# Kernel tuning notes

Hardware: AMD Instinct MI355X
Metric: run time of the kernel (lower is better)

Reference implementation:

```python
import jax, jax.numpy as jnp
import numpy as np

D_MODEL = 1024
NHEAD = 16
HEAD_DIM = D_MODEL // NHEAD
B, S = 8, 1024
NEG = -1e9  # finite stand-in for -inf (same softmax result, grad-safe)


def setup_inputs() -> dict:
    key = jax.random.key(0)
    ks = jax.random.split(key, 12)
    sc = 1.0 / np.sqrt(D_MODEL)
    inp = {
        "q": jax.random.normal(ks[0], (B, S, D_MODEL), jnp.float32),
        "k": jax.random.normal(ks[1], (B, S, D_MODEL), jnp.float32),
        "v": jax.random.normal(ks[2], (B, S, D_MODEL), jnp.float32),
        "padding_mask": jax.random.bernoulli(ks[3], 0.1, (B, S)),
        "causal_mask": jnp.where(jnp.tril(jnp.ones((S, S), bool)), 0.0, NEG).astype(jnp.float32),
        "wq": jax.random.normal(ks[4], (D_MODEL, D_MODEL), jnp.float32) * sc,
        "bq": jax.random.normal(ks[5], (D_MODEL,), jnp.float32) * sc,
        "wk": jax.random.normal(ks[6], (D_MODEL, D_MODEL), jnp.float32) * sc,
        "wv": jax.random.normal(ks[7], (D_MODEL, D_MODEL), jnp.float32) * sc,
        "bv": jax.random.normal(ks[8], (D_MODEL,), jnp.float32) * sc,
        "wo": jax.random.normal(ks[9], (D_MODEL, D_MODEL), jnp.float32) * sc,
        "bo": jax.random.normal(ks[10], (D_MODEL,), jnp.float32) * sc,
    }
    return inp


def reference(q, k, v, padding_mask, causal_mask, wq, bq, wk, wv, bv, wo, bo):
    b = q.shape[0]
    # projections (torch Linear: x @ W.T + b); k_linear has no bias
    qp = q @ wq.T + bq
    kp = k @ wk.T
    vp = v @ wv.T + bv
    # [B, S, H, Dh] -> [B, H, S, Dh]
    qh = qp.reshape(b, -1, NHEAD, HEAD_DIM).transpose(0, 2, 1, 3)
    kh = kp.reshape(b, -1, NHEAD, HEAD_DIM).transpose(0, 2, 1, 3)
    vh = vp.reshape(b, -1, NHEAD, HEAD_DIM).transpose(0, 2, 1, 3)
    scores = jnp.einsum("bhqd,bhkd->bhqk", qh, kh) / np.sqrt(HEAD_DIM).astype(np.float32)
    scores = jnp.where(padding_mask[:, None, None, :], NEG, scores)
    scores = scores + causal_mask[None, None, :, :]
    attn = jax.nn.softmax(scores, axis=-1)
    out = jnp.einsum("bhqk,bhkd->bhqd", attn, vh)
    out = out.transpose(0, 2, 1, 3).reshape(b, -1, D_MODEL)
    return out @ wo.T + bo
```

## Files before the change

kernel.cpp:

```cpp
#include <hip/hip_runtime.h>
#include <hip/hip_bf16.h>
#include <cstdint>
#include <math.h>


typedef __bf16 bf16_t;
typedef __bf16 bf16x8 __attribute__((ext_vector_type(8)));
typedef __bf16 bf16x4 __attribute__((ext_vector_type(4)));
typedef float  f32x4  __attribute__((ext_vector_type(4)));

#define MFMA16(a, b, c) __builtin_amdgcn_mfma_f32_16x16x32_bf16((a), (b), (c), 0, 0, 0)
#define NEGV (-1e9f)

__device__ __forceinline__ void gl_lds16(const void* gp, void* lp) {
  __builtin_amdgcn_global_load_lds(
      (__attribute__((address_space(1))) void*)(gp),
      (__attribute__((address_space(3))) void*)(lp), 16, 0, 0);
}

__device__ __forceinline__ void bar() {
  asm volatile("" ::: "memory");
  __builtin_amdgcn_s_barrier();
  asm volatile("" ::: "memory");
}

__device__ __forceinline__ unsigned int pk2(float lo, float hi) {
  unsigned short a = __builtin_bit_cast(unsigned short, (bf16_t)lo);
  unsigned short b = __builtin_bit_cast(unsigned short, (bf16_t)hi);
  return (unsigned int)a | ((unsigned int)b << 16);
}

__device__ __forceinline__ void cvt_body(const float* __restrict__ in,
                                         bf16_t* __restrict__ out, int i) {
  const float4* p = reinterpret_cast<const float4*>(in) + (size_t)i * 2;
  float4 a = p[0], b = p[1];
  bf16x8 r = {(bf16_t)a.x, (bf16_t)a.y, (bf16_t)a.z, (bf16_t)a.w,
              (bf16_t)b.x, (bf16_t)b.y, (bf16_t)b.z, (bf16_t)b.w};
  *reinterpret_cast<bf16x8*>(out + (size_t)i * 8) = r;
}

__global__ __launch_bounds__(256) void cvt_all(
    const float* __restrict__ q, const float* __restrict__ k, const float* __restrict__ v,
    const float* __restrict__ wq, const float* __restrict__ wk,
    const float* __restrict__ wv, const float* __restrict__ wo,
    bf16_t* __restrict__ oq, bf16_t* __restrict__ ok, bf16_t* __restrict__ ov,
    bf16_t* __restrict__ owq, bf16_t* __restrict__ owk,
    bf16_t* __restrict__ owv, bf16_t* __restrict__ owo) {
  const int bid = (int)blockIdx.x;
  if (bid < 12288) {
    const int s = bid >> 12;
    const int i = (bid & 4095) * 256 + (int)threadIdx.x;
    cvt_body(s == 0 ? q : (s == 1 ? k : v),
             s == 0 ? oq : (s == 1 ? ok : ov), i);
  } else {
    const int r = bid - 12288;
    const int s = r >> 9;
    const int i = (r & 511) * 256 + (int)threadIdx.x;
    cvt_body(s == 0 ? wq : (s == 1 ? wk : (s == 2 ? wv : wo)),
             s == 0 ? owq : (s == 1 ? owk : (s == 2 ? owv : owo)), i);
  }
}


#define GEMM_KLOOP(Ag, Wg, lds, acc, lr, lg, wr, wc)                          \
  auto stageA = [&](int buf, int tile) {                                      \
    char* dst = lds + buf * 32768 + t * 16;                                   \
    const size_t kt = (size_t)tile * 64;                                      \
    gl_lds16(Ag + kt,                    dst);                                \
    gl_lds16(Ag + kt + (size_t)64 * K,   dst + 8192);                         \
    gl_lds16(Ag + kt + (size_t)128 * K,  dst + 16384);                        \
    gl_lds16(Ag + kt + (size_t)192 * K,  dst + 24576);                        \
  };                                                                          \
  auto stageB = [&](int buf, int tile) {                                      \
    char* dst = lds + 98304 + buf * 16384 + t * 16;                           \
    const size_t kt = (size_t)tile * 64;                                      \
    gl_lds16(Wg + kt,                    dst);                                \
    gl_lds16(Wg + kt + (size_t)64 * K,   dst + 8192);                         \
  };                                                                          \
  stageA(0, 0); stageB(0, 0); stageA(1, 1); stageB(1, 1);                     \
  asm volatile("s_waitcnt vmcnt(6)" ::: "memory");   \
  bar();                                                      \
  const int xorv = (lr & 7) << 4;                                             \
  const int k0o = lg * 16, k1o = 64 + lg * 16;                                \
  for (int T = 0; T < 16; ++T) {                                              \
    const int cur = T % 3;                                                    \
    const char* Ab = lds + cur * 32768;                                       \
    const char* Bb = lds + 98304 + cur * 16384;                               \
    bf16x8 af[4][2], b0[2][2], b1[2][2];                                      \
                                \
    _Pragma("unroll")                                                         \
    for (int mt = 0; mt < 4; mt++) {                                          \
      const int row = wr * 64 + mt * 16 + lr;                                 \
      af[mt][0] = *(const bf16x8*)(Ab + row * 128 + (k0o ^ xorv));            \
      af[mt][1] = *(const bf16x8*)(Ab + row * 128 + (k1o ^ xorv));            \
    }                                                                         \
    _Pragma("unroll")                                                         \
    for (int nt = 0; nt < 2; nt++) {                                          \
      const int row = wc * 64 + nt * 16 + lr;                                 \
      b0[nt][0] = *(const bf16x8*)(Bb + row * 128 + (k0o ^ xorv));            \
      b0[nt][1] = *(const bf16x8*)(Bb + row * 128 + (k1o ^ xorv));            \
    }                                                                         \
    if (T + 2 < 16) stageA((T + 2) % 3, T + 2);                               \
    bar();                                                                    \
    asm volatile("s_waitcnt lgkmcnt(0)" ::: "memory");                        \
    __builtin_amdgcn_s_setprio(1);                                            \
    _Pragma("unroll")                                                         \
    for (int mt = 0; mt < 4; mt++)                                            \
      _Pragma("unroll")                                                       \
      for (int nt = 0; nt < 2; nt++) {                                        \
        acc[mt][nt] = MFMA16(af[mt][0], b0[nt][0], acc[mt][nt]);              \
        acc[mt][nt] = MFMA16(af[mt][1], b0[nt][1], acc[mt][nt]);              \
      }                                                                       \
    __builtin_amdgcn_s_setprio(0);                                            \
    bar();                                                                    \
            \
    _Pragma("unroll")                                                         \
    for (int nt = 0; nt < 2; nt++) {                                          \
      const int row = wc * 64 + (nt + 2) * 16 + lr;                           \
      b1[nt][0] = *(const bf16x8*)(Bb + row * 128 + (k0o ^ xorv));            \
      b1[nt][1] = *(const bf16x8*)(Bb + row * 128 + (k1o ^ xorv));            \
    }                                                                         \
    if (T + 2 < 16) stageB((T + 2) % 3, T + 2);                               \
    if (T < 14)       asm volatile("s_waitcnt vmcnt(6)" ::: "memory");        \
    else if (T == 14) asm volatile("s_waitcnt vmcnt(0)" ::: "memory");        \
    bar();                                     \
    asm volatile("s_waitcnt lgkmcnt(0)" ::: "memory");                        \
    __builtin_amdgcn_s_setprio(1);                                            \
    _Pragma("unroll")                                                         \
    for (int mt = 0; mt < 4; mt++)                                            \
      _Pragma("unroll")                                                       \
      for (int nt = 0; nt < 2; nt++) {                                        \
        acc[mt][nt + 2] = MFMA16(af[mt][0], b1[nt][0], acc[mt][nt + 2]);      \
        acc[mt][nt + 2] = MFMA16(af[mt][1], b1[nt][1], acc[mt][nt + 2]);      \
      }                                                                       \
    __builtin_amdgcn_s_setprio(0);                                            \
    bar();                                                                    \
  }

__global__ __launch_bounds__(512) void gemm_qkv(const bf16_t* __restrict__ qbf,
                                                const bf16_t* __restrict__ kbf,
                                                const bf16_t* __restrict__ vbf,
                                                const bf16_t* __restrict__ wqb,
                                                const bf16_t* __restrict__ wkb,
                                                const bf16_t* __restrict__ wvb,
                                                const float* __restrict__ bq,
                                                const float* __restrict__ bv,
                                                bf16_t* __restrict__ qp,
                                                bf16_t* __restrict__ kp,
                                                bf16_t* __restrict__ vtw) {
  __shared__ __align__(16) char lds[147456];
  const int bid = (int)blockIdx.x;
  const int z = bid >> 8;
  const int idx = bid & 255;
  const int p = ((idx >> 6) << 3) | (idx & 7);
  const int n = (idx >> 3) & 7;
  const bf16_t* A = z == 0 ? qbf : (z == 1 ? kbf : vbf);
  const bf16_t* W = z == 0 ? wqb : (z == 1 ? wkb : wvb);
  const int t = threadIdx.x;
  const int w = t >> 6, l = t & 63, lr = l & 15, lg = l >> 4;
  const int wr = w >> 1, wc = w & 1;
  const int m0 = p * 256, n0 = n * 128;
  const int K = 1024, N = 1024;

  const int gc = (t & 7) ^ ((t >> 3) & 7);
  const bf16_t* Ag = A + (size_t)(m0 + (t >> 3)) * K + gc * 8;
  const bf16_t* Wg = W + (size_t)(n0 + (t >> 3)) * K + gc * 8;

  f32x4 acc[4][4] = {};
  GEMM_KLOOP(Ag, Wg, lds, acc, lr, lg, wr, wc)

  if (z != 2) {
    bf16_t* outp = (z == 0) ? qp : kp;
    const float sc = (z == 0) ? 0.125f : 1.0f;
#pragma unroll
    for (int nt = 0; nt < 4; nt++) {
      const int col = n0 + wc * 64 + nt * 16 + lr;
      const float bb = (z == 0) ? bq[col] : 0.0f;
#pragma unroll
      for (int mt = 0; mt < 4; mt++)
#pragma unroll
        for (int i = 0; i < 4; i++) {
          const int row = m0 + wr * 64 + mt * 16 + lg * 4 + i;
          outp[(size_t)row * N + col] = (bf16_t)((acc[mt][nt][i] + bb) * sc);
        }
    }
  } else {
    __syncthreads();
    char* Tl = lds;
#pragma unroll
    for (int nt = 0; nt < 4; nt++) {
      const int col_l = wc * 64 + nt * 16 + lr;
      const float bb = bv[n0 + col_l];
#pragma unroll
      for (int mt = 0; mt < 4; mt++)
#pragma unroll
        for (int i = 0; i < 4; i++) {
          const int row_l = wr * 64 + mt * 16 + lg * 4 + i;
          *(bf16_t*)(Tl + col_l * 512 + ((row_l * 2) ^ ((col_l & 7) << 4))) =
              (bf16_t)(acc[mt][nt][i] + bb);
        }
    }
    __syncthreads();
    const int b = m0 >> 10, s0 = m0 & 1023;
    const int c_l = t >> 2, sub = t & 3;
    bf16_t* dst = vtw + (size_t)(b * 1024 + n0 + c_l) * 1024 + s0 + sub * 64;
    const char* Trow = Tl + c_l * 512;
    const int sw2 = (c_l & 7) << 4;
#pragma unroll
    for (int jj = 0; jj < 8; jj++) {
      const int lc = sub * 8 + jj;
      bf16x8 vv = *(const bf16x8*)(Trow + ((lc << 4) ^ sw2));
      *(bf16x8*)(dst + jj * 8) = vv;
    }
  }
}

__global__ __launch_bounds__(512) void gemm_out(const bf16_t* __restrict__ A,
                                                const bf16_t* __restrict__ W,
                                                const float* __restrict__ bias,
                                                float* __restrict__ outp) {
  __shared__ __align__(16) char lds[147456];
  const int bid = (int)blockIdx.x;
  const int p = ((bid >> 6) << 3) | (bid & 7);
  const int n = (bid >> 3) & 7;
  const int t = threadIdx.x;
  const int w = t >> 6, l = t & 63, lr = l & 15, lg = l >> 4;
  const int wr = w >> 1, wc = w & 1;
  const int m0 = p * 256, n0 = n * 128;
  const int K = 1024, N = 1024;

  const int gc = (t & 7) ^ ((t >> 3) & 7);
  const bf16_t* Ag = A + (size_t)(m0 + (t >> 3)) * K + gc * 8;
  const bf16_t* Wg = W + (size_t)(n0 + (t >> 3)) * K + gc * 8;

  f32x4 acc[4][4] = {};
  GEMM_KLOOP(Ag, Wg, lds, acc, lr, lg, wr, wc)

#pragma unroll
  for (int nt = 0; nt < 4; nt++) {
    const int col = n0 + wc * 64 + nt * 16 + lr;
    const float bb = bias[col];
#pragma unroll
    for (int mt = 0; mt < 4; mt++)
#pragma unroll
      for (int i = 0; i < 4; i++) {
        const int row = m0 + wr * 64 + mt * 16 + lg * 4 + i;
        outp[(size_t)row * N + col] = acc[mt][nt][i] + bb;
      }
  }
}

__device__ __forceinline__ void pack_bfly(const f32x4 (&s)[4], int lg,
                                          bf16x8& pbv0, bf16x8& pbv1) {
  unsigned int u[4][2], sh[4][2];
#pragma unroll
  for (int nt = 0; nt < 4; nt++) {
    u[nt][0] = pk2(s[nt][0], s[nt][1]);
    u[nt][1] = pk2(s[nt][2], s[nt][3]);
  }
#pragma unroll
  for (int nt = 0; nt < 4; nt++) {
    sh[nt][0] = (unsigned int)__shfl_xor((int)u[nt][0], 16, 64);
    sh[nt][1] = (unsigned int)__shfl_xor((int)u[nt][1], 16, 64);
  }
  const bool ev = (lg & 1) == 0;
  unsigned int Y[8];
  Y[0] = ev ? u[0][0] : sh[1][0];  Y[1] = ev ? u[0][1] : sh[1][1];
  Y[2] = ev ? u[2][0] : sh[3][0];  Y[3] = ev ? u[2][1] : sh[3][1];
  Y[4] = ev ? sh[0][0] : u[1][0];  Y[5] = ev ? sh[0][1] : u[1][1];
  Y[6] = ev ? sh[2][0] : u[3][0];  Y[7] = ev ? sh[2][1] : u[3][1];
  const bool mid = (lg == 1) || (lg == 2);
#pragma unroll
  for (int j = 0; j < 8; j++) {
    const unsigned int z = (unsigned int)__shfl_xor((int)Y[j], 48, 64);
    Y[j] = mid ? z : Y[j];
  }
  union U8 { unsigned int u[4]; bf16x8 v; };
  U8 p0, p1;
  p0.u[0] = Y[0]; p0.u[1] = Y[1]; p0.u[2] = Y[4]; p0.u[3] = Y[5];
  p1.u[0] = Y[2]; p1.u[1] = Y[3]; p1.u[2] = Y[6]; p1.u[3] = Y[7];
  pbv0 = p0.v;
  pbv1 = p1.v;
}

__global__ __launch_bounds__(512, 8) void attn_fused(const bf16_t* __restrict__ qp,
                                                     const bf16_t* __restrict__ kp,
                                                     const bf16_t* __restrict__ vt,
                                                     const int* __restrict__ pad,
                                                     bf16_t* __restrict__ outp) {
  __shared__ bf16_t Ks[2][64 * 64];
  __shared__ bf16_t Vts[2][64 * 64];
  __shared__ int padI[1024];
  __shared__ int sfl[8], sfh[8];
  const int t = threadIdx.x, w = t >> 6, l = t & 63, lr = l & 15, lg = l >> 4;
  const int L = (int)blockIdx.x;
  const int bh = (L & 7) + ((L >> 6) << 3);
  const int j = (L >> 3) & 7;
  const int b = bh >> 4, h = bh & 15;
  const int lo = j, hi = 15 - j;

  const int srow = t >> 3, sc = t & 7;
  const int gc = sc ^ (srow & 7);
  const bf16_t* kgb = kp + (size_t)(b * 1024 + srow) * 1024 + h * 64 + gc * 8;
  const bf16_t* vgb = vt + (size_t)(bh * 64 + srow) * 1024 + gc * 8;

  auto stage = [&](int bufi, int k0s) {
    gl_lds16(kgb + (size_t)k0s * 1024, (char*)(Ks[bufi]) + t * 16);
    gl_lds16(vgb + k0s,                (char*)(Vts[bufi]) + t * 16);
  };

  bool unl = false, unh = false;
  for (int jj = t; jj <= hi * 64; jj += 512) {
    const bool u = (pad[b * 1024 + jj] == 0);
    unh |= u;
    unl |= (u && (jj <= lo * 64));
  }
  const bool al = __any(unl), ah = __any(unh);
  if (l == 0) { sfl[w] = al ? 1 : 0; sfh[w] = ah ? 1 : 0; }

  stage(0, 0);
  if (t < 256) gl_lds16(pad + b * 1024 + t * 4, (char*)padI + t * 16);

  const int mytile = (w < 4) ? hi : lo;
  const int qrow_l = mytile * 64 + (w & 3) * 16 + lr;
  const int base16 = mytile * 64 + (w & 3) * 16;
  const bf16_t* qg = qp + (size_t)(b * 1024 + qrow_l) * 1024 + h * 64 + lg * 8;
  const bf16x8 qa0 = *reinterpret_cast<const bf16x8*>(qg);
  const bf16x8 qa1 = *reinterpret_cast<const bf16x8*>(qg + 32);

  __syncthreads();
  int ul = 0, uh = 0;
#pragma unroll
  for (int i = 0; i < 8; i++) { ul |= sfl[i]; uh |= sfh[i]; }
  const bool mydeg = (w < 4) ? (uh == 0) : (ul == 0);
  const int ktEnd = (ul == 0) ? 16 : (hi + 1);

  f32x4 o[4] = {};
  float m_ = -INFINITY, ld_ = 0.0f;

  for (int kt = 0; kt < ktEnd; ++kt) {
    const int cur = kt & 1;
    if (kt + 1 < ktEnd) {
      stage(cur ^ 1, (kt + 1) * 64);
      asm volatile("s_waitcnt vmcnt(2)" ::: "memory");
    } else {
      asm volatile("s_waitcnt vmcnt(0)" ::: "memory");
    }
    __builtin_amdgcn_s_barrier();

    if (kt <= mytile || mydeg) {
      const char* Kb = (const char*)(Ks[cur]);
      const char* Vb = (const char*)(Vts[cur]);
      const int k0 = kt * 64;

      f32x4 s[4] = {};
#pragma unroll
      for (int nt = 0; nt < 4; nt++) {
        const int row = nt * 16 + lr;
        const int sw = (row & 7) << 4;
        bf16x8 kb0 = *reinterpret_cast<const bf16x8*>(Kb + row * 128 + ((lg * 16) ^ sw));
        bf16x8 kb1 = *reinterpret_cast<const bf16x8*>(Kb + row * 128 + ((lg * 16 + 64) ^ sw));
        s[nt] = MFMA16(kb0, qa0, s[nt]);
        s[nt] = MFMA16(kb1, qa1, s[nt]);
      }

      const bool nc = (k0 + 63 > base16);
#pragma unroll
      for (int nt = 0; nt < 4; nt++) {
        const int kc4 = k0 + nt * 16 + lg * 4;
        const int4 pd = *reinterpret_cast<const int4*>(&padI[kc4]);
        const int pdv[4] = {pd.x, pd.y, pd.z, pd.w};
#pragma unroll
        for (int i = 0; i < 4; i++) {
          float v = s[nt][i];
          if (pdv[i]) v = NEGV;
          if (nc && (kc4 + i > qrow_l)) v += NEGV;
          s[nt][i] = v;
        }
      }

      float mx = s[0][0];
#pragma unroll
      for (int nt = 0; nt < 4; nt++)
#pragma unroll
        for (int i = 0; i < 4; i++) mx = fmaxf(mx, s[nt][i]);
      mx = fmaxf(mx, __shfl_xor(mx, 16, 64));
      mx = fmaxf(mx, __shfl_xor(mx, 32, 64));

      if (!__all(mx <= m_ - 88.0f)) {
        if (!__all(mx <= m_ + 8.0f)) {
          const float mn = fmaxf(m_, mx);
          const float scl = __expf(m_ - mn);
          m_ = mn;
          ld_ *= scl;
#pragma unroll
          for (int nt = 0; nt < 4; nt++) o[nt] *= scl;
        }
        float a = 0.0f;
#pragma unroll
        for (int nt = 0; nt < 4; nt++)
#pragma unroll
          for (int i = 0; i < 4; i++) {
            const float p = __expf(s[nt][i] - m_);
            s[nt][i] = p;
            a += p;
          }
        a += __shfl_xor(a, 16, 64);
        a += __shfl_xor(a, 32, 64);
        ld_ += a;

        bf16x8 pb0, pb1;
        pack_bfly(s, lg, pb0, pb1);

#pragma unroll
        for (int nt = 0; nt < 4; nt++) {
          const int vrow = nt * 16 + lr;
          const int vsw = (vrow & 7) << 4;
          bf16x8 vf0 = *reinterpret_cast<const bf16x8*>(Vb + vrow * 128 + ((lg * 16) ^ vsw));
          bf16x8 vf1 = *reinterpret_cast<const bf16x8*>(Vb + vrow * 128 + ((64 + lg * 16) ^ vsw));
          o[nt] = MFMA16(vf0, pb0, o[nt]);
          o[nt] = MFMA16(vf1, pb1, o[nt]);
        }
      }
    }
    __builtin_amdgcn_s_barrier();
  }

  const float rinv = 1.0f / ld_;
#pragma unroll
  for (int nt = 0; nt < 4; nt++) {
    bf16x4 rr = {(bf16_t)(o[nt][0] * rinv), (bf16_t)(o[nt][1] * rinv),
                 (bf16_t)(o[nt][2] * rinv), (bf16_t)(o[nt][3] * rinv)};
    *reinterpret_cast<bf16x4*>(outp + (size_t)(b * 1024 + qrow_l) * 1024 + h * 64 + nt * 16 + lg * 4) = rr;
  }
}

extern "C" void kernel_launch(void* const* d_in, const int* in_sizes, int n_in,
                              void* d_out, int out_size, void* d_ws, size_t ws_size,
                              hipStream_t stream) {
  const float* q   = (const float*)d_in[0];
  const float* k   = (const float*)d_in[1];
  const float* v   = (const float*)d_in[2];
  const int*   pad = (const int*)d_in[3];
  const float* wq  = (const float*)d_in[5];
  const float* bq  = (const float*)d_in[6];
  const float* wk  = (const float*)d_in[7];
  const float* wv  = (const float*)d_in[8];
  const float* bv  = (const float*)d_in[9];
  const float* wo  = (const float*)d_in[10];
  const float* bo  = (const float*)d_in[11];

  char* ws = (char*)d_ws;
  const size_t MiB = 1024 * 1024;
  bf16_t* qbf = (bf16_t*)(ws + 0 * MiB);
  bf16_t* kbf = (bf16_t*)(ws + 16 * MiB);
  bf16_t* vbf = (bf16_t*)(ws + 32 * MiB);
  bf16_t* qp  = (bf16_t*)(ws + 48 * MiB);
  bf16_t* kp  = (bf16_t*)(ws + 64 * MiB);
  bf16_t* vtw = (bf16_t*)(ws + 80 * MiB);
  bf16_t* wqb = (bf16_t*)(ws + 96 * MiB);
  bf16_t* wkb = (bf16_t*)(ws + 98 * MiB);
  bf16_t* wvb = (bf16_t*)(ws + 100 * MiB);
  bf16_t* wob = (bf16_t*)(ws + 102 * MiB);
  bf16_t* attnO = qbf;

  cvt_all<<<14336, 256, 0, stream>>>(q, k, v, wq, wk, wv, wo,
                                     qbf, kbf, vbf, wqb, wkb, wvb, wob);

  gemm_qkv<<<768, 512, 0, stream>>>(qbf, kbf, vbf, wqb, wkb, wvb, bq, bv, qp, kp, vtw);

  attn_fused<<<1024, 512, 0, stream>>>(qp, kp, vtw, pad, attnO);

  gemm_out<<<256, 512, 0, stream>>>(attnO, wob, bo, (float*)d_out);
}
```

Before: 174.1 us.

## Fuse fp32-to-bf16 activation conversion into QKV projection GEMM A-loads

Result: slower. 191.1 us (+9.7%).

```diff
diff --git a/kernel.cpp b/kernel.cpp
--- a/kernel.cpp
+++ b/kernel.cpp
@@ -39,55 +39,99 @@
   *reinterpret_cast<bf16x8*>(out + (size_t)i * 8) = r;
 }
 
-__global__ __launch_bounds__(256) void cvt_all(
-    const float* __restrict__ q, const float* __restrict__ k, const float* __restrict__ v,
+__global__ __launch_bounds__(256) void cvt_w(
     const float* __restrict__ wq, const float* __restrict__ wk,
     const float* __restrict__ wv, const float* __restrict__ wo,
-    bf16_t* __restrict__ oq, bf16_t* __restrict__ ok, bf16_t* __restrict__ ov,
     bf16_t* __restrict__ owq, bf16_t* __restrict__ owk,
     bf16_t* __restrict__ owv, bf16_t* __restrict__ owo) {
   const int bid = (int)blockIdx.x;
-  if (bid < 12288) {
-    const int s = bid >> 12;
-    const int i = (bid & 4095) * 256 + (int)threadIdx.x;
-    cvt_body(s == 0 ? q : (s == 1 ? k : v),
-             s == 0 ? oq : (s == 1 ? ok : ov), i);
-  } else {
-    const int r = bid - 12288;
-    const int s = r >> 9;
-    const int i = (r & 511) * 256 + (int)threadIdx.x;
-    cvt_body(s == 0 ? wq : (s == 1 ? wk : (s == 2 ? wv : wo)),
-             s == 0 ? owq : (s == 1 ? owk : (s == 2 ? owv : owo)), i);
-  }
-}
-
-
-#define GEMM_KLOOP(Ag, Wg, lds, acc, lr, lg, wr, wc)                          \
-  auto stageA = [&](int buf, int tile) {                                      \
-    char* dst = lds + buf * 32768 + t * 16;                                   \
-    const size_t kt = (size_t)tile * 64;                                      \
-    gl_lds16(Ag + kt,                    dst);                                \
-    gl_lds16(Ag + kt + (size_t)64 * K,   dst + 8192);                         \
-    gl_lds16(Ag + kt + (size_t)128 * K,  dst + 16384);                        \
-    gl_lds16(Ag + kt + (size_t)192 * K,  dst + 24576);                        \
-  };                                                                          \
-  auto stageB = [&](int buf, int tile) {                                      \
-    char* dst = lds + 98304 + buf * 16384 + t * 16;                           \
-    const size_t kt = (size_t)tile * 64;                                      \
-    gl_lds16(Wg + kt,                    dst);                                \
-    gl_lds16(Wg + kt + (size_t)64 * K,   dst + 8192);                         \
-  };                                                                          \
-  stageA(0, 0); stageB(0, 0); stageA(1, 1); stageB(1, 1);                     \
-  asm volatile("s_waitcnt vmcnt(6)" ::: "memory");   \
-  bar();                                                      \
-  const int xorv = (lr & 7) << 4;                                             \
-  const int k0o = lg * 16, k1o = 64 + lg * 16;                                \
-  for (int T = 0; T < 16; ++T) {                                              \
-    const int cur = T % 3;                                                    \
-    const char* Ab = lds + cur * 32768;                                       \
-    const char* Bb = lds + 98304 + cur * 16384;                               \
+  const int s = bid >> 9;
+  const int i = (bid & 511) * 256 + (int)threadIdx.x;
+  cvt_body(s == 0 ? wq : (s == 1 ? wk : (s == 2 ? wv : wo)),
+           s == 0 ? owq : (s == 1 ? owk : (s == 2 ? owv : owo)), i);
+}
+
+
+struct AReg { float4 v[8]; };
+
+__device__ __forceinline__ void loadA_f32(const float* __restrict__ Agf,
+                                          int tile, AReg& g) {
+  const size_t kt = (size_t)tile * 64;
+#pragma unroll
+  for (int rr = 0; rr < 4; rr++) {
+    const float* src = Agf + (size_t)(rr * 64) * 1024 + kt;
+    g.v[rr * 2]     = *(const float4*)(src);
+    g.v[rr * 2 + 1] = *(const float4*)(src + 4);
+  }
+}
+
+__device__ __forceinline__ void cvtWriteA(char* ldsA, int t, const AReg& g) {
+#pragma unroll
+  for (int rr = 0; rr < 4; rr++) {
+    float4 a = g.v[rr * 2], b = g.v[rr * 2 + 1];
+    bf16x8 r = {(bf16_t)a.x, (bf16_t)a.y, (bf16_t)a.z, (bf16_t)a.w,
+                (bf16_t)b.x, (bf16_t)b.y, (bf16_t)b.z, (bf16_t)b.w};
+    *(bf16x8*)(ldsA + rr * 8192 + t * 16) = r;
+  }
+}
+
+__global__ __launch_bounds__(512) void gemm_qkv(const float* __restrict__ qf,
+                                                const float* __restrict__ kf,
+                                                const float* __restrict__ vf,
+                                                const bf16_t* __restrict__ wqb,
+                                                const bf16_t* __restrict__ wkb,
+                                                const bf16_t* __restrict__ wvb,
+                                                const float* __restrict__ bq,
+                                                const float* __restrict__ bv,
+                                                bf16_t* __restrict__ qp,
+                                                bf16_t* __restrict__ kp,
+                                                bf16_t* __restrict__ vtw) {
+  __shared__ __align__(16) char lds[114688];
+  const int bid = (int)blockIdx.x;
+  const int z = bid >> 8;
+  const int idx = bid & 255;
+  const int p = ((idx >> 6) << 3) | (idx & 7);
+  const int n = (idx >> 3) & 7;
+  const float*  A = z == 0 ? qf : (z == 1 ? kf : vf);
+  const bf16_t* W = z == 0 ? wqb : (z == 1 ? wkb : wvb);
+  const int t = threadIdx.x;
+  const int w = t >> 6, l = t & 63, lr = l & 15, lg = l >> 4;
+  const int wr = w >> 1, wc = w & 1;
+  const int m0 = p * 256, n0 = n * 128;
+  const int K = 1024, N = 1024;
+
+  const int gc = (t & 7) ^ ((t >> 3) & 7);
+  const float*  Agf = A + (size_t)(m0 + (t >> 3)) * K + gc * 8;
+  const bf16_t* Wg  = W + (size_t)(n0 + (t >> 3)) * K + gc * 8;
+
+  auto stageB = [&](int buf, int tile) {
+    char* dst = lds + 65536 + buf * 16384 + t * 16;
+    const size_t kt = (size_t)tile * 64;
+    gl_lds16(Wg + kt,                  dst);
+    gl_lds16(Wg + kt + (size_t)64 * K, dst + 8192);
+  };
+
+  AReg g0, g1;
+  loadA_f32(Agf, 0, g0);
+  stageB(0, 0);
+  loadA_f32(Agf, 1, g1);
+  stageB(1, 1);
+  asm volatile("s_waitcnt vmcnt(12)" ::: "memory");
+  cvtWriteA(lds, t, g0);
+  asm volatile("s_waitcnt vmcnt(10)" ::: "memory");
+  asm volatile("s_waitcnt lgkmcnt(0)" ::: "memory");
+  bar();
+
+  f32x4 acc[4][4] = {};
+  const int xorv = (lr & 7) << 4;
+  const int k0o = lg * 16, k1o = 64 + lg * 16;
+
+#define QKV_ITER(T, gIssue, gCvt)                                             \
+  {                                                                           \
+    const char* Ab = lds + ((T) & 1) * 32768;                                 \
+    const char* Bb = lds + 65536 + ((T) % 3) * 16384;                         \
     bf16x8 af[4][2], b0[2][2], b1[2][2];                                      \
-                                \
+                              \
     _Pragma("unroll")                                                         \
     for (int mt = 0; mt < 4; mt++) {                                          \
       const int row = wr * 64 + mt * 16 + lr;                                 \
@@ -100,7 +144,7 @@
       b0[nt][0] = *(const bf16x8*)(Bb + row * 128 + (k0o ^ xorv));            \
       b0[nt][1] = *(const bf16x8*)(Bb + row * 128 + (k1o ^ xorv));            \
     }                                                                         \
-    if (T + 2 < 16) stageA((T + 2) % 3, T + 2);                               \
+    if ((T) + 2 < 16) loadA_f32(Agf, (T) + 2, gIssue);                        \
     bar();                                                                    \
     asm volatile("s_waitcnt lgkmcnt(0)" ::: "memory");                        \
     __builtin_amdgcn_s_setprio(1);                                            \
@@ -113,18 +157,19 @@
       }                                                                       \
     __builtin_amdgcn_s_setprio(0);                                            \
     bar();                                                                    \
-            \
+       \
     _Pragma("unroll")                                                         \
     for (int nt = 0; nt < 2; nt++) {                                          \
       const int row = wc * 64 + (nt + 2) * 16 + lr;                           \
       b1[nt][0] = *(const bf16x8*)(Bb + row * 128 + (k0o ^ xorv));            \
       b1[nt][1] = *(const bf16x8*)(Bb + row * 128 + (k1o ^ xorv));            \
     }                                                                         \
-    if (T + 2 < 16) stageB((T + 2) % 3, T + 2);                               \
-    if (T < 14)       asm volatile("s_waitcnt vmcnt(6)" ::: "memory");        \
-    else if (T == 14) asm volatile("s_waitcnt vmcnt(0)" ::: "memory");        \
-    bar();                                     \
+    if ((T) + 2 < 16) stageB(((T) + 2) % 3, (T) + 2);                         \
+    if ((T) < 14)       asm volatile("s_waitcnt vmcnt(10)" ::: "memory");     \
+    else if ((T) == 14) asm volatile("s_waitcnt vmcnt(0)" ::: "memory");      \
+    if ((T) + 1 < 16) cvtWriteA(lds + (((T) + 1) & 1) * 32768, t, gCvt);      \
     asm volatile("s_waitcnt lgkmcnt(0)" ::: "memory");                        \
+    bar();                                                                    \
     __builtin_amdgcn_s_setprio(1);                                            \
     _Pragma("unroll")                                                         \
     for (int mt = 0; mt < 4; mt++)                                            \
@@ -137,37 +182,12 @@
     bar();                                                                    \
   }
 
-__global__ __launch_bounds__(512) void gemm_qkv(const bf16_t* __restrict__ qbf,
-                                                const bf16_t* __restrict__ kbf,
-                                                const bf16_t* __restrict__ vbf,
-                                                const bf16_t* __restrict__ wqb,
-                                                const bf16_t* __restrict__ wkb,
-                                                const bf16_t* __restrict__ wvb,
-                                                const float* __restrict__ bq,
-                                                const float* __restrict__ bv,
-                                                bf16_t* __restrict__ qp,
-                                                bf16_t* __restrict__ kp,
-                                                bf16_t* __restrict__ vtw) {
-  __shared__ __align__(16) char lds[147456];
-  const int bid = (int)blockIdx.x;
-  const int z = bid >> 8;
-  const int idx = bid & 255;
-  const int p = ((idx >> 6) << 3) | (idx & 7);
-  const int n = (idx >> 3) & 7;
-  const bf16_t* A = z == 0 ? qbf : (z == 1 ? kbf : vbf);
-  const bf16_t* W = z == 0 ? wqb : (z == 1 ? wkb : wvb);
-  const int t = threadIdx.x;
-  const int w = t >> 6, l = t & 63, lr = l & 15, lg = l >> 4;
-  const int wr = w >> 1, wc = w & 1;
-  const int m0 = p * 256, n0 = n * 128;
-  const int K = 1024, N = 1024;
-
-  const int gc = (t & 7) ^ ((t >> 3) & 7);
-  const bf16_t* Ag = A + (size_t)(m0 + (t >> 3)) * K + gc * 8;
-  const bf16_t* Wg = W + (size_t)(n0 + (t >> 3)) * K + gc * 8;
-
-  f32x4 acc[4][4] = {};
-  GEMM_KLOOP(Ag, Wg, lds, acc, lr, lg, wr, wc)
+#pragma unroll 1
+  for (int TT = 0; TT < 16; TT += 2) {
+    QKV_ITER(TT, g0, g1)
+    QKV_ITER(TT + 1, g1, g0)
+  }
+#undef QKV_ITER
 
   if (z != 2) {
     bf16_t* outp = (z == 0) ? qp : kp;
@@ -233,8 +253,80 @@
   const bf16_t* Ag = A + (size_t)(m0 + (t >> 3)) * K + gc * 8;
   const bf16_t* Wg = W + (size_t)(n0 + (t >> 3)) * K + gc * 8;
 
+  auto stageA = [&](int buf, int tile) {
+    char* dst = lds + buf * 32768 + t * 16;
+    const size_t kt = (size_t)tile * 64;
+    gl_lds16(Ag + kt,                    dst);
+    gl_lds16(Ag + kt + (size_t)64 * K,   dst + 8192);
+    gl_lds16(Ag + kt + (size_t)128 * K,  dst + 16384);
+    gl_lds16(Ag + kt + (size_t)192 * K,  dst + 24576);
+  };
+  auto stageB = [&](int buf, int tile) {
+    char* dst = lds + 98304 + buf * 16384 + t * 16;
+    const size_t kt = (size_t)tile * 64;
+    gl_lds16(Wg + kt,                    dst);
+    gl_lds16(Wg + kt + (size_t)64 * K,   dst + 8192);
+  };
+  stageA(0, 0); stageB(0, 0); stageA(1, 1); stageB(1, 1);
+  asm volatile("s_waitcnt vmcnt(6)" ::: "memory");
+  bar();
+
   f32x4 acc[4][4] = {};
-  GEMM_KLOOP(Ag, Wg, lds, acc, lr, lg, wr, wc)
+  const int xorv = (lr & 7) << 4;
+  const int k0o = lg * 16, k1o = 64 + lg * 16;
+
+  for (int T = 0; T < 16; ++T) {
+    const int cur = T % 3;
+    const char* Ab = lds + cur * 32768;
+    const char* Bb = lds + 98304 + cur * 16384;
+    bf16x8 af[4][2], b0[2][2], b1[2][2];
+#pragma unroll
+    for (int mt = 0; mt < 4; mt++) {
+      const int row = wr * 64 + mt * 16 + lr;
+      af[mt][0] = *(const bf16x8*)(Ab + row * 128 + (k0o ^ xorv));
+      af[mt][1] = *(const bf16x8*)(Ab + row * 128 + (k1o ^ xorv));
+    }
+#pragma unroll
+    for (int nt = 0; nt < 2; nt++) {
+      const int row = wc * 64 + nt * 16 + lr;
+      b0[nt][0] = *(const bf16x8*)(Bb + row * 128 + (k0o ^ xorv));
+      b0[nt][1] = *(const bf16x8*)(Bb + row * 128 + (k1o ^ xorv));
+    }
+    if (T + 2 < 16) stageA((T + 2) % 3, T + 2);
+    bar();
+    asm volatile("s_waitcnt lgkmcnt(0)" ::: "memory");
+    __builtin_amdgcn_s_setprio(1);
+#pragma unroll
+    for (int mt = 0; mt < 4; mt++)
+#pragma unroll
+      for (int nt = 0; nt < 2; nt++) {
+        acc[mt][nt] = MFMA16(af[mt][0], b0[nt][0], acc[mt][nt]);
+        acc[mt][nt] = MFMA16(af[mt][1], b0[nt][1], acc[mt][nt]);
+      }
+    __builtin_amdgcn_s_setprio(0);
+    bar();
+#pragma unroll
+    for (int nt = 0; nt < 2; nt++) {
+      const int row = wc * 64 + (nt + 2) * 16 + lr;
+      b1[nt][0] = *(const bf16x8*)(Bb + row * 128 + (k0o ^ xorv));
+      b1[nt][1] = *(const bf16x8*)(Bb + row * 128 + (k1o ^ xorv));
+    }
+    if (T + 2 < 16) stageB((T + 2) % 3, T + 2);
+    if (T < 14)       asm volatile("s_waitcnt vmcnt(6)" ::: "memory");
+    else if (T == 14) asm volatile("s_waitcnt vmcnt(0)" ::: "memory");
+    bar();
+    asm volatile("s_waitcnt lgkmcnt(0)" ::: "memory");
+    __builtin_amdgcn_s_setprio(1);
+#pragma unroll
+    for (int mt = 0; mt < 4; mt++)
+#pragma unroll
+      for (int nt = 0; nt < 2; nt++) {
+        acc[mt][nt + 2] = MFMA16(af[mt][0], b1[nt][0], acc[mt][nt + 2]);
+        acc[mt][nt + 2] = MFMA16(af[mt][1], b1[nt][1], acc[mt][nt + 2]);
+      }
+    __builtin_amdgcn_s_setprio(0);
+    bar();
+  }
 
 #pragma unroll
   for (int nt = 0; nt < 4; nt++) {
@@ -452,9 +544,7 @@
 
   char* ws = (char*)d_ws;
   const size_t MiB = 1024 * 1024;
-  bf16_t* qbf = (bf16_t*)(ws + 0 * MiB);
-  bf16_t* kbf = (bf16_t*)(ws + 16 * MiB);
-  bf16_t* vbf = (bf16_t*)(ws + 32 * MiB);
+  bf16_t* attnO = (bf16_t*)(ws + 0 * MiB);
   bf16_t* qp  = (bf16_t*)(ws + 48 * MiB);
   bf16_t* kp  = (bf16_t*)(ws + 64 * MiB);
   bf16_t* vtw = (bf16_t*)(ws + 80 * MiB);
@@ -462,12 +552,10 @@
   bf16_t* wkb = (bf16_t*)(ws + 98 * MiB);
   bf16_t* wvb = (bf16_t*)(ws + 100 * MiB);
   bf16_t* wob = (bf16_t*)(ws + 102 * MiB);
-  bf16_t* attnO = qbf;
-
-  cvt_all<<<14336, 256, 0, stream>>>(q, k, v, wq, wk, wv, wo,
-                                     qbf, kbf, vbf, wqb, wkb, wvb, wob);
-
-  gemm_qkv<<<768, 512, 0, stream>>>(qbf, kbf, vbf, wqb, wkb, wvb, bq, bv, qp, kp, vtw);
+
+  cvt_w<<<2048, 256, 0, stream>>>(wq, wk, wv, wo, wqb, wkb, wvb, wob);
+
+  gemm_qkv<<<768, 512, 0, stream>>>(q, k, v, wqb, wkb, wvb, bq, bv, qp, kp, vtw);
 
   attn_fused<<<1024, 512, 0, stream>>>(qp, kp, vtw, pad, attnO);
 
```
